# Optimization experiments

Hardware: AMD Instinct MI355X
Metric: run time of the kernel (lower is better)

The kernel has to match this reference:

```python
import jax, jax.numpy as jnp
import numpy as np

N_BLADES = 8      # 2**len(sig_g), sig_g=[1,1,1]
N_EP_STEPS = 3
STEP_SIZE = 0.01
B, IN_DIM, OUT_DIM = 1024, 4096, 2048
HID = OUT_DIM * N_BLADES


def setup_inputs() -> dict:
    key = jax.random.key(0)
    k0, k1, k2, k3, k4, k5 = jax.random.split(key, 6)
    x = jax.random.normal(k0, (B, IN_DIM), jnp.float32)
    # input_proj: Linear(in_dim, out_dim*n_blades)
    W_in = jax.random.normal(k1, (IN_DIM, HID), jnp.float32) / np.sqrt(IN_DIM)
    b_in = jax.random.normal(k2, (HID,), jnp.float32) * 0.01
    # energy interaction matrix W: (n_blades, n_blades), init * 0.1
    W_e = jax.random.normal(k3, (N_BLADES, N_BLADES), jnp.float32) * 0.1
    # output_proj: Linear(out_dim*n_blades, out_dim)
    W_out = jax.random.normal(k4, (HID, OUT_DIM), jnp.float32) / np.sqrt(HID)
    b_out = jax.random.normal(k5, (OUT_DIM,), jnp.float32) * 0.01
    return {"x": x, "W_in": W_in, "b_in": b_in, "W_e": W_e,
            "W_out": W_out, "b_out": b_out}


def reference(x, W_in, b_in, W_e, W_out, b_out):
    # h: (B, out_dim, n_blades)
    h = (x @ W_in + b_in).reshape(x.shape[0], OUT_DIM, N_BLADES)
    # EP relaxation: analytic dE/dh = h + 0.1 * h @ (W + W^T)
    # (torch computed this via autograd on a detached copy each step,
    #  so the gradient term carries no graph -> stop_gradient)
    W_sym = W_e + W_e.T
    for _ in range(N_EP_STEPS):
        grad = jax.lax.stop_gradient(h + 0.1 * (h @ W_sym))
        h = h - STEP_SIZE * grad
    h_flat = h.reshape(x.shape[0], HID)
    return h_flat @ W_out + b_out
```

## Files before the change

kernel.cpp:

```cpp
#include <hip/hip_runtime.h>
#include <stdint.h>

#define AS1 __attribute__((address_space(1)))
#define AS3 __attribute__((address_space(3)))

typedef float v4f __attribute__((ext_vector_type(4)));
typedef __bf16 v8bf __attribute__((ext_vector_type(8)));
typedef __bf16 bf16x4 __attribute__((ext_vector_type(4)));

static_assert(sizeof(v8bf) == 16, "v8bf must be 16B");
static_assert(sizeof(bf16x4) == 8, "bf16x4 must be 8B");

__device__ __forceinline__ unsigned short f2bf(float f) {
  unsigned int x = __float_as_uint(f);
  x += 0x7fffu + ((x >> 16) & 1u);
  return (unsigned short)(x >> 16);
}

__device__ __forceinline__ float bf2f(unsigned short u) {
  return __uint_as_float((unsigned int)u << 16);
}

__device__ __forceinline__ void async16(void* lds, const void* g) {
  __builtin_amdgcn_global_load_lds((const AS1 unsigned int*)g,
                                   (AS3 unsigned int*)lds, 16, 0, 0);
}


__global__ void prep_m3_kernel(const float* __restrict__ We, float* __restrict__ m3) {
  __shared__ float Ms[64], M2[64];
  int t = threadIdx.x;
  int i = t >> 3, j = t & 7;
  float wsym = We[i * 8 + j] + We[j * 8 + i];
  Ms[t] = (i == j ? 0.99f : 0.0f) - 0.001f * wsym;
  __syncthreads();
  float s = 0.f;
#pragma unroll
  for (int p = 0; p < 8; ++p) s += Ms[i * 8 + p] * Ms[p * 8 + j];
  M2[t] = s;
  __syncthreads();
  s = 0.f;
#pragma unroll
  for (int p = 0; p < 8; ++p) s += M2[i * 8 + p] * Ms[p * 8 + j];
  m3[t] = s;
}

__global__ void cvt_bf16_kernel(const float* __restrict__ in, unsigned short* __restrict__ out) {
  int i = (blockIdx.x * 256 + threadIdx.x) * 8;
  float4 a = *(const float4*)(in + i);
  float4 b = *(const float4*)(in + i + 4);
  alignas(16) unsigned short r[8] = {f2bf(a.x), f2bf(a.y), f2bf(a.z), f2bf(a.w),
                                     f2bf(b.x), f2bf(b.y), f2bf(b.z), f2bf(b.w)};
  *(uint4*)(out + i) = *(const uint4*)r;
}

template <bool OUT_BF16, bool SPLITK, bool FOLD>
__global__ __launch_bounds__(512, 1) void gemm256f_kernel(
    const unsigned short* __restrict__ A, const float* __restrict__ Bsrc,
    const float* __restrict__ bias, void* __restrict__ Cout,
    int M, int N, int K, int ldkA, int ldnB, const float* __restrict__ m3) {
  __shared__ char ldsc[131072];

  const int flat = blockIdx.x + gridDim.x * (blockIdx.y + gridDim.y * blockIdx.z);
  const int xcd = flat & 7, idx = flat >> 3;
  int bn, bm, bz;
  if (SPLITK) { bz = xcd; bn = idx & 7; bm = idx >> 3; }
  else        { bz = 0;   bn = xcd * 8 + (idx & 7); bm = idx >> 3; }
  const int m0 = bm * 256, n0 = bn * 256;
  const int kb = SPLITK ? bz * K : 0;

  const int t = threadIdx.x;
  const int lane = t & 63, w = t >> 6;
  const int wr = w >> 2, wn = w & 3;
  const int r16 = lane & 15, kc = lane >> 4;
  const int xorv = (r16 & 7) << 4;
  const int acol0 = (kc << 4) ^ xorv;
  const int acol1 = ((4 | kc) << 4) ^ xorv;
  const int abase = wr * 16384 + r16 * 128;
  const int bbase = 32768 + wn * 8192 + r16 * 128;

  const int srow = w * 8 + (lane >> 3);
  const int scol = ((lane & 7) ^ (lane >> 3)) * 8;
  const int sdst = w * 1024 + lane * 16;
  const unsigned short* gAp = A + (size_t)(m0 + srow) * ldkA + kb + scol;

  const int n0s = 4 * lane;
  const int rotc = (lane >> 1) & 3;
  const float* gB = Bsrc + (size_t)(kb + w * 4) * ldnB + n0 + n0s;

  v4f acc[8][4];
#pragma unroll
  for (int mi = 0; mi < 8; ++mi)
#pragma unroll
    for (int nj = 0; nj < 4; ++nj) acc[mi][nj] = (v4f){0.f, 0.f, 0.f, 0.f};

  float4 L[2][4];

#define STAGE_A(OB)                                                        \
  _Pragma("unroll") for (int i = 0; i < 4; ++i)                            \
      async16(ldsc + (OB) + i * 8192 + sdst, gAp + (size_t)(i * 64) * ldkA);
#define LOAD_BGLB()                                                        \
  _Pragma("unroll") for (int ii = 0; ii < 2; ++ii)                         \
      _Pragma("unroll") for (int j = 0; j < 4; ++j)                        \
          L[ii][j] = *(const float4*)(gB + (size_t)(ii * 32 + j) * ldnB);
#define CVT_WRITE_B(OB)                                                          \
  _Pragma("unroll") for (int ii = 0; ii < 2; ++ii) {                             \
    const int k4 = w * 4 + ii * 32;                                              \
    bf16x4 R0 = (bf16x4){(__bf16)L[ii][0].x, (__bf16)L[ii][1].x,                 \
                         (__bf16)L[ii][2].x, (__bf16)L[ii][3].x};                \
    bf16x4 R1 = (bf16x4){(__bf16)L[ii][0].y, (__bf16)L[ii][1].y,                 \
                         (__bf16)L[ii][2].y, (__bf16)L[ii][3].y};                \
    bf16x4 R2 = (bf16x4){(__bf16)L[ii][0].z, (__bf16)L[ii][1].z,                 \
                         (__bf16)L[ii][2].z, (__bf16)L[ii][3].z};                \
    bf16x4 R3 = (bf16x4){(__bf16)L[ii][0].w, (__bf16)L[ii][1].w,                 \
                         (__bf16)L[ii][2].w, (__bf16)L[ii][3].w};                \
    _Pragma("unroll") for (int d = 0; d < 4; ++d) {                              \
      int o = (d + rotc) & 3;                                                    \
      int row = n0s + o;                                                         \
      bf16x4 vv = (o & 2) ? ((o & 1) ? R3 : R2) : ((o & 1) ? R1 : R0);           \
      *(bf16x4*)(ldsc + (OB) + 32768 + row * 128 +                               \
                 ((((k4 >> 3) ^ (row & 7)) << 4) | ((k4 & 7) << 1))) = vv;       \
    }                                                                            \
  }
#define LOAD_A(BB, MH)                                                     \
  _Pragma("unroll") for (int m = 0; m < 4; ++m) {                          \
    a[m * 2 + 0] = *(const v8bf*)(ldsc + (BB) + abase + (MH) * 8192 + m * 2048 + acol0); \
    a[m * 2 + 1] = *(const v8bf*)(ldsc + (BB) + abase + (MH) * 8192 + m * 2048 + acol1); \
  }
#define LOAD_B(BB, NH, BR)                                                 \
  _Pragma("unroll") for (int n = 0; n < 2; ++n) {                          \
    BR[n * 2 + 0] = *(const v8bf*)(ldsc + (BB) + bbase + (NH) * 4096 + n * 2048 + acol0); \
    BR[n * 2 + 1] = *(const v8bf*)(ldsc + (BB) + bbase + (NH) * 4096 + n * 2048 + acol1); \
  }
#define MFMA_QUAD(MH, NH, BR)                                              \
  _Pragma("unroll") for (int m = 0; m < 4; ++m) {                          \
    _Pragma("unroll") for (int n = 0; n < 2; ++n) {                        \
      acc[(MH) * 4 + m][(NH) * 2 + n] = __builtin_amdgcn_mfma_f32_16x16x32_bf16( \
          a[m * 2 + 0], BR[n * 2 + 0], acc[(MH) * 4 + m][(NH) * 2 + n], 0, 0, 0); \
      acc[(MH) * 4 + m][(NH) * 2 + n] = __builtin_amdgcn_mfma_f32_16x16x32_bf16( \
          a[m * 2 + 1], BR[n * 2 + 1], acc[(MH) * 4 + m][(NH) * 2 + n], 0, 0, 0); \
    }                                                                      \
  }

  const int NT = K >> 6;

  STAGE_A(0);
  LOAD_BGLB();
  gAp += 64;
  CVT_WRITE_B(0);
  if (NT > 1) gB += (size_t)64 * ldnB;
  LOAD_BGLB();
  if (NT > 2) gB += (size_t)64 * ldnB;
  asm volatile("s_waitcnt lgkmcnt(0)" ::: "memory");
  __builtin_amdgcn_s_barrier();

  int buf = 0;
  for (int tt = 0; tt < NT; ++tt) {
    const int bb = buf << 16;
    const int ob = (buf ^ 1) << 16;
    const bool pf = (tt + 1 < NT);

    if (pf) { STAGE_A(ob); gAp += 64; }
    __builtin_amdgcn_sched_barrier(0);

    {
      v8bf a[8], b0r[4], b1r[4];
      LOAD_A(bb, 0);
      LOAD_B(bb, 0, b0r);
      LOAD_B(bb, 1, b1r);
      MFMA_QUAD(0, 0, b0r);
      MFMA_QUAD(0, 1, b1r);
      __builtin_amdgcn_sched_barrier(0);

      LOAD_A(bb, 1);
      if (pf) { CVT_WRITE_B(ob); }
      LOAD_BGLB();
      if (tt + 3 < NT) gB += (size_t)64 * ldnB;
      __builtin_amdgcn_sched_barrier(0);

      MFMA_QUAD(1, 1, b1r);
      MFMA_QUAD(1, 0, b0r);
    }
    __builtin_amdgcn_sched_barrier(0);

    asm volatile("s_waitcnt vmcnt(8) lgkmcnt(0)" ::: "memory");
    __builtin_amdgcn_s_barrier();
    buf ^= 1;
  }

  if (FOLD) {
#pragma unroll
    for (int mi = 0; mi < 8; ++mi) {
      int lrow = wr * 128 + mi * 16 + kc * 4;
#pragma unroll
      for (int nj = 0; nj < 4; ++nj) {
        int lcol = wn * 64 + nj * 16 + r16;
        float bv = bias[n0 + lcol];
#pragma unroll
        for (int j = 0; j < 4; ++j)
          *(unsigned short*)(ldsc + (lrow + j) * 512 + lcol * 2) =
              f2bf(acc[mi][nj][j] + bv);
      }
    }
    __syncthreads();
    float m3r[64];
#pragma unroll
    for (int p = 0; p < 64; ++p) m3r[p] = m3[p];
    const int cg = (t & 31) * 8;
    const int rof = (t >> 5);
    unsigned short* ho = (unsigned short*)Cout;
#pragma unroll
    for (int pass = 0; pass < 16; ++pass) {
      int row = pass * 16 + rof;
      uint4 raw = *(const uint4*)(ldsc + row * 512 + cg * 2);
      const unsigned short* rp = (const unsigned short*)&raw;
      float v[8];
#pragma unroll
      for (int p = 0; p < 8; ++p) v[p] = bf2f(rp[p]);
      alignas(16) unsigned short o[8];
#pragma unroll
      for (int j = 0; j < 8; ++j) {
        float s = 0.f;
#pragma unroll
        for (int p = 0; p < 8; ++p) s += v[p] * m3r[p * 8 + j];
        o[j] = f2bf(s);
      }
      *(uint4*)(ho + (size_t)(m0 + row) * N + n0 + cg) = *(const uint4*)o;
    }
    return;
  }

  unsigned short* Pp =
      (unsigned short*)Cout + (SPLITK ? (size_t)bz * M * N : 0);
#pragma unroll
  for (int mi = 0; mi < 8; ++mi) {
    int grow = m0 + wr * 128 + mi * 16 + kc * 4;
#pragma unroll
    for (int nj = 0; nj < 4; ++nj) {
      int gcol = n0 + wn * 64 + nj * 16 + r16;
      float bv = SPLITK ? 0.f : bias[gcol];
#pragma unroll
      for (int j = 0; j < 4; ++j) {
        float v = acc[mi][nj][j] + bv;
        size_t idxo = (size_t)(grow + j) * N + gcol;
        if (OUT_BF16)
          ((unsigned short*)Cout)[idxo] = f2bf(v);
        else if (SPLITK)
          Pp[idxo] = f2bf(v);
        else
          ((float*)Cout)[idxo] = v;
      }
    }
  }
#undef STAGE_A
#undef LOAD_BGLB
#undef CVT_WRITE_B
#undef LOAD_A
#undef LOAD_B
#undef MFMA_QUAD
}

__global__ void reduce_splitk_kernel(const unsigned short* __restrict__ part,
                                     const float* __restrict__ bias,
                                     float* __restrict__ out, int MN, int N, int S) {
  int i = (blockIdx.x * 256 + threadIdx.x) * 4;
  float4 s = {0.f, 0.f, 0.f, 0.f};
  for (int k = 0; k < S; ++k) {
    ushort4 v = *(const ushort4*)(part + (size_t)k * MN + i);
    s.x += bf2f(v.x); s.y += bf2f(v.y); s.z += bf2f(v.z); s.w += bf2f(v.w);
  }
  int n = i & (N - 1);
  const float4 bv = *(const float4*)(bias + n);
  s.x += bv.x; s.y += bv.y; s.z += bv.z; s.w += bv.w;
  *(float4*)(out + i) = s;
}


extern "C" void kernel_launch(void* const* d_in, const int* in_sizes, int n_in,
                              void* d_out, int out_size, void* d_ws, size_t ws_size,
                              hipStream_t stream) {
  const float* x     = (const float*)d_in[0];
  const float* W_in  = (const float*)d_in[1];
  const float* b_in  = (const float*)d_in[2];
  const float* W_e   = (const float*)d_in[3];
  const float* W_out = (const float*)d_in[4];
  const float* b_out = (const float*)d_in[5];
  float* out = (float*)d_out;

  char* ws = (char*)d_ws;
  const size_t OFF_M3 = 0;
  const size_t OFF_X  = 1ull << 20;
  const size_t OFF_H  = 10ull << 20;
  const size_t OFF_P  = 48ull << 20;
  float* m3          = (float*)(ws + OFF_M3);
  unsigned short* xb = (unsigned short*)(ws + OFF_X);
  unsigned short* h  = (unsigned short*)(ws + OFF_H);
  unsigned short* part = (unsigned short*)(ws + OFF_P);

  prep_m3_kernel<<<1, 64, 0, stream>>>(W_e, m3);
  cvt_bf16_kernel<<<2048, 256, 0, stream>>>(x, xb);

  gemm256f_kernel<true, false, true><<<dim3(64, 4), 512, 0, stream>>>(
      xb, W_in, b_in, h, 1024, 16384, 4096, 4096, 16384, m3);

  gemm256f_kernel<false, true, false><<<dim3(8, 4, 8), 512, 0, stream>>>(
      h, W_out, nullptr, part, 1024, 2048, 2048, 16384, 2048, nullptr);

  reduce_splitk_kernel<<<2048, 256, 0, stream>>>(part, b_out, out, 1024 * 2048, 2048, 8);
}
```

Baseline: 232.7 us.

## Switch GEMM inner loop from 16x16x32 to 32x32x16 bf16 MFMA

Replaces the 16x16x32 bf16 MFMA tiles with 32x32x16 tiles, so each wave holds 4x2 blocks of 16-float accumulators instead of 8x4 blocks of 4-float ones. LDS fragment addressing and both epilogues (the fold path and the plain store path) are remapped to the 32x32 output layout. The larger MFMA gives more math per LDS fragment read and fewer instructions issued. In exchange the phasing changes: each half of the loop now covers a K-half rather than an N-half, and the epilogue stores become more scattered.

```diff
diff --git a/kernel.cpp b/kernel.cpp
--- a/kernel.cpp
+++ b/kernel.cpp
@@ -5,6 +5,7 @@
 #define AS3 __attribute__((address_space(3)))
 
 typedef float v4f __attribute__((ext_vector_type(4)));
+typedef float f32x16 __attribute__((ext_vector_type(16)));
 typedef __bf16 v8bf __attribute__((ext_vector_type(8)));
 typedef __bf16 bf16x4 __attribute__((ext_vector_type(4)));
 
@@ -72,12 +73,12 @@
   const int t = threadIdx.x;
   const int lane = t & 63, w = t >> 6;
   const int wr = w >> 2, wn = w & 3;
-  const int r16 = lane & 15, kc = lane >> 4;
-  const int xorv = (r16 & 7) << 4;
-  const int acol0 = (kc << 4) ^ xorv;
-  const int acol1 = ((4 | kc) << 4) ^ xorv;
-  const int abase = wr * 16384 + r16 * 128;
-  const int bbase = 32768 + wn * 8192 + r16 * 128;
+  const int l31 = lane & 31, l7 = lane & 7, ln5 = lane >> 5;
+  int acol32[4];
+#pragma unroll
+  for (int kk = 0; kk < 4; ++kk) acol32[kk] = (((kk * 2 + ln5) ^ l7) << 4);
+  const int abase = wr * 16384 + l31 * 128;
+  const int bbase = 32768 + wn * 8192 + l31 * 128;
 
   const int srow = w * 8 + (lane >> 3);
   const int scol = ((lane & 7) ^ (lane >> 3)) * 8;
@@ -88,11 +89,13 @@
   const int rotc = (lane >> 1) & 3;
   const float* gB = Bsrc + (size_t)(kb + w * 4) * ldnB + n0 + n0s;
 
-  v4f acc[8][4];
-#pragma unroll
-  for (int mi = 0; mi < 8; ++mi)
-#pragma unroll
-    for (int nj = 0; nj < 4; ++nj) acc[mi][nj] = (v4f){0.f, 0.f, 0.f, 0.f};
+  f32x16 acc[4][2];
+#pragma unroll
+  for (int mi = 0; mi < 4; ++mi)
+#pragma unroll
+    for (int nj = 0; nj < 2; ++nj)
+#pragma unroll
+      for (int e = 0; e < 16; ++e) acc[mi][nj][e] = 0.f;
 
   float4 L[2][4];
 
@@ -122,25 +125,22 @@
                  ((((k4 >> 3) ^ (row & 7)) << 4) | ((k4 & 7) << 1))) = vv;       \
     }                                                                            \
   }
-#define LOAD_A(BB, MH)                                                     \
-  _Pragma("unroll") for (int m = 0; m < 4; ++m) {                          \
-    a[m * 2 + 0] = *(const v8bf*)(ldsc + (BB) + abase + (MH) * 8192 + m * 2048 + acol0); \
-    a[m * 2 + 1] = *(const v8bf*)(ldsc + (BB) + abase + (MH) * 8192 + m * 2048 + acol1); \
-  }
-#define LOAD_B(BB, NH, BR)                                                 \
-  _Pragma("unroll") for (int n = 0; n < 2; ++n) {                          \
-    BR[n * 2 + 0] = *(const v8bf*)(ldsc + (BB) + bbase + (NH) * 4096 + n * 2048 + acol0); \
-    BR[n * 2 + 1] = *(const v8bf*)(ldsc + (BB) + bbase + (NH) * 4096 + n * 2048 + acol1); \
-  }
-#define MFMA_QUAD(MH, NH, BR)                                              \
-  _Pragma("unroll") for (int m = 0; m < 4; ++m) {                          \
-    _Pragma("unroll") for (int n = 0; n < 2; ++n) {                        \
-      acc[(MH) * 4 + m][(NH) * 2 + n] = __builtin_amdgcn_mfma_f32_16x16x32_bf16( \
-          a[m * 2 + 0], BR[n * 2 + 0], acc[(MH) * 4 + m][(NH) * 2 + n], 0, 0, 0); \
-      acc[(MH) * 4 + m][(NH) * 2 + n] = __builtin_amdgcn_mfma_f32_16x16x32_bf16( \
-          a[m * 2 + 1], BR[n * 2 + 1], acc[(MH) * 4 + m][(NH) * 2 + n], 0, 0, 0); \
-    }                                                                      \
-  }
+#define LOAD_A(BB, KH)                                                     \
+  _Pragma("unroll") for (int m = 0; m < 4; ++m)                            \
+    _Pragma("unroll") for (int q = 0; q < 2; ++q)                          \
+      a[m * 2 + q] = *(const v8bf*)(ldsc + (BB) + abase + m * 4096 +       \
+                                    acol32[(KH) * 2 + q]);
+#define LOAD_B(BB, KH, BR)                                                 \
+  _Pragma("unroll") for (int n = 0; n < 2; ++n)                            \
+    _Pragma("unroll") for (int q = 0; q < 2; ++q)                          \
+      BR[n * 2 + q] = *(const v8bf*)(ldsc + (BB) + bbase + n * 4096 +      \
+                                     acol32[(KH) * 2 + q]);
+#define MFMA_HALF(BR)                                                      \
+  _Pragma("unroll") for (int m = 0; m < 4; ++m)                            \
+    _Pragma("unroll") for (int n = 0; n < 2; ++n)                          \
+      _Pragma("unroll") for (int q = 0; q < 2; ++q)                        \
+        acc[m][n] = __builtin_amdgcn_mfma_f32_32x32x16_bf16(               \
+            a[m * 2 + q], BR[n * 2 + q], acc[m][n], 0, 0, 0);
 
   const int NT = K >> 6;
 
@@ -168,8 +168,7 @@
       LOAD_A(bb, 0);
       LOAD_B(bb, 0, b0r);
       LOAD_B(bb, 1, b1r);
-      MFMA_QUAD(0, 0, b0r);
-      MFMA_QUAD(0, 1, b1r);
+      MFMA_HALF(b0r);
       __builtin_amdgcn_sched_barrier(0);
 
       LOAD_A(bb, 1);
@@ -178,8 +177,7 @@
       if (tt + 3 < NT) gB += (size_t)64 * ldnB;
       __builtin_amdgcn_sched_barrier(0);
 
-      MFMA_QUAD(1, 1, b1r);
-      MFMA_QUAD(1, 0, b0r);
+      MFMA_HALF(b1r);
     }
     __builtin_amdgcn_sched_barrier(0);
 
@@ -190,16 +188,18 @@
 
   if (FOLD) {
 #pragma unroll
-    for (int mi = 0; mi < 8; ++mi) {
-      int lrow = wr * 128 + mi * 16 + kc * 4;
-#pragma unroll
-      for (int nj = 0; nj < 4; ++nj) {
-        int lcol = wn * 64 + nj * 16 + r16;
+    for (int mf = 0; mf < 4; ++mf) {
+      int rbase = wr * 128 + mf * 32 + 4 * ln5;
+#pragma unroll
+      for (int nf = 0; nf < 2; ++nf) {
+        int lcol = wn * 64 + nf * 32 + l31;
         float bv = bias[n0 + lcol];
 #pragma unroll
-        for (int j = 0; j < 4; ++j)
-          *(unsigned short*)(ldsc + (lrow + j) * 512 + lcol * 2) =
-              f2bf(acc[mi][nj][j] + bv);
+        for (int j = 0; j < 16; ++j) {
+          int lrow = rbase + (j & 3) + 8 * (j >> 2);
+          *(unsigned short*)(ldsc + lrow * 512 + lcol * 2) =
+              f2bf(acc[mf][nf][j] + bv);
+        }
       }
     }
     __syncthreads();
@@ -233,16 +233,17 @@
   unsigned short* Pp =
       (unsigned short*)Cout + (SPLITK ? (size_t)bz * M * N : 0);
 #pragma unroll
-  for (int mi = 0; mi < 8; ++mi) {
-    int grow = m0 + wr * 128 + mi * 16 + kc * 4;
-#pragma unroll
-    for (int nj = 0; nj < 4; ++nj) {
-      int gcol = n0 + wn * 64 + nj * 16 + r16;
+  for (int mf = 0; mf < 4; ++mf) {
+    int grow = m0 + wr * 128 + mf * 32 + 4 * ln5;
+#pragma unroll
+    for (int nf = 0; nf < 2; ++nf) {
+      int gcol = n0 + wn * 64 + nf * 32 + l31;
       float bv = SPLITK ? 0.f : bias[gcol];
 #pragma unroll
-      for (int j = 0; j < 4; ++j) {
-        float v = acc[mi][nj][j] + bv;
-        size_t idxo = (size_t)(grow + j) * N + gcol;
+      for (int j = 0; j < 16; ++j) {
+        int row = grow + (j & 3) + 8 * (j >> 2);
+        float v = acc[mf][nf][j] + bv;
+        size_t idxo = (size_t)row * N + gcol;
         if (OUT_BF16)
           ((unsigned short*)Cout)[idxo] = f2bf(v);
         else if (SPLITK)
@@ -257,7 +258,7 @@
 #undef CVT_WRITE_B
 #undef LOAD_A
 #undef LOAD_B
-#undef MFMA_QUAD
+#undef MFMA_HALF
 }
 
 __global__ void reduce_splitk_kernel(const unsigned short* __restrict__ part,
```

Measured after the change: 247.2 us. 1.06x slower.
